# Optimization experiments

Measured on AMD Instinct MI355X. Metric: run time of the kernel, lower is better.

## Reference

```python
import jax, jax.numpy as jnp
import numpy as np

ALPHA = 0.2  # LeakyReLU negative slope


def setup_inputs() -> dict:
    key = jax.random.key(0)
    ks = jax.random.split(key, 6)
    B, N, F_in, F_out, H = 16, 1024, 256, 256, 8
    h = jax.random.normal(ks[0], (B, N, F_in), dtype=jnp.float32)
    # Per-head Linear W: weight [F_out, F_in] + bias [F_out], stacked over heads
    W = jax.random.normal(ks[1], (H, F_out, F_in), dtype=jnp.float32) * (1.414 / np.sqrt(F_in))
    bW = jax.random.normal(ks[2], (H, F_out), dtype=jnp.float32) * 0.01
    # Per-head Linear A: weight [1, 2*F_out] split into a1 (acts on Whi) and a2 (acts on Whj), bias bA [1]
    a1 = jax.random.normal(ks[3], (H, F_out), dtype=jnp.float32) * (1.414 / np.sqrt(2 * F_out))
    a2 = jax.random.normal(ks[4], (H, F_out), dtype=jnp.float32) * (1.414 / np.sqrt(2 * F_out))
    bA = jax.random.normal(ks[5], (H,), dtype=jnp.float32) * 0.01
    return {"h": h, "W": W, "bW": bW, "a1": a1, "a2": a2, "bA": bA}


def reference(h, W, bW, a1, a2, bA):
    # h: [B,N,F_in], W: [H,F_out,F_in]
    B, N, _ = h.shape
    H, F_out, _ = W.shape
    Wh = jnp.einsum('bnf,hof->bhno', h, W) + bW[None, :, None, :]  # [B,H,N,F_out]
    # Additive score e_ij = a1.Wh_i + a2.Wh_j + bA  (decomposed; avoids N x N x 2F concat)
    ei = jnp.einsum('bhno,ho->bhn', Wh, a1)  # contribution of row node i
    ej = jnp.einsum('bhno,ho->bhn', Wh, a2)  # contribution of col node j
    e = ei[:, :, :, None] + ej[:, :, None, :] + bA[None, :, None, None]  # [B,H,N,N]
    e = jnp.where(e > 0, e, ALPHA * e)  # LeakyReLU
    att = jax.nn.softmax(e, axis=-1)  # softmax over neighbors j (dropout = identity in eval)
    aWh = jnp.einsum('bhij,bhjo->bhio', att, Wh)  # [B,H,N,F_out]
    out = jax.nn.relu(aWh)  # last=False branch
    out = out.transpose(0, 2, 1, 3).reshape(B, N, H * F_out)  # concat heads on feature dim
    return jax.nn.sigmoid(out)
```

## Files before the change

### kernel.cpp

```cpp
#include <hip/hip_runtime.h>


#define L2E 1.442695041f

typedef _Float16 half8 __attribute__((ext_vector_type(8)));
typedef __fp16 fp16x2 __attribute__((ext_vector_type(2)));
typedef float floatx4 __attribute__((ext_vector_type(4)));

#if __has_builtin(__builtin_amdgcn_exp2f)
#define EXP2F(x) __builtin_amdgcn_exp2f(x)
#else
#define EXP2F(x) exp2f(x)
#endif

static __device__ inline unsigned int pack2(float a, float b) {
    fp16x2 h = __builtin_amdgcn_cvt_pkrtz(a, b);
    return __builtin_bit_cast(unsigned int, h);
}

static __device__ inline int swz(int row, int c) {
    return (row << 6) + ((((c) ^ (row >> 1)) & 3) << 4);
}
static __device__ inline int swz128(int row, int c) {
    return (row << 7) + ((((c) ^ row) & 7) << 4);
}

__global__ __launch_bounds__(256, 3) void wh_kernel(
    const float* __restrict__ hin, const float* __restrict__ W,
    const float* __restrict__ bW, _Float16* __restrict__ WhT,
    const float* __restrict__ a1, const float* __restrict__ a2,
    float* __restrict__ eiP, float* __restrict__ ejP)
{
    const int bnt  = blockIdx.x;
    const int ot   = blockIdx.y;
    const int head = blockIdx.z;
    const int t    = threadIdx.x;
    const int wave = t >> 6, lane = t & 63;
    const int l15 = lane & 15, quad = lane >> 4;
    const int wmh = wave & 1, wnh = wave >> 1;

    __shared__ char smem[16384];
    _Float16* As = (_Float16*)smem;
    _Float16* Bs = (_Float16*)(smem + 8192);
    float* bWs   = (float*)smem;
    float* a1s   = (float*)(smem + 512);
    float* a2s   = (float*)(smem + 1024);
    float* part1 = (float*)(smem + 1536);
    float* part2 = (float*)(smem + 2560);

    const int o0 = ot * 128;
    const int bn0 = bnt * 128;
    floatx4 acc[4][4];
#pragma unroll
    for (int a = 0; a < 4; a++)
#pragma unroll
        for (int b = 0; b < 4; b++) acc[a][b] = (floatx4)0.0f;

    const int ar = t >> 1, ah = t & 1;
    const float* Wrow = W + (size_t)(head * 256 + o0 + ar) * 256 + ah * 16;
    const float* hrow = hin + (size_t)(bn0 + ar) * 256 + ah * 16;

    float4 pa0, pa1, pa2, pa3, pb0, pb1, pb2, pb3;
    {
        const float4* p4 = (const float4*)Wrow;
        pa0 = p4[0]; pa1 = p4[1]; pa2 = p4[2]; pa3 = p4[3];
        const float4* q4 = (const float4*)hrow;
        pb0 = q4[0]; pb1 = q4[1]; pb2 = q4[2]; pb3 = q4[3];
    }

    for (int f0 = 0; f0 < 256; f0 += 32) {
        __syncthreads();
        *(uint4*)((char*)As + swz(ar, 2 * ah)) =
            make_uint4(pack2(pa0.x, pa0.y), pack2(pa0.z, pa0.w),
                       pack2(pa1.x, pa1.y), pack2(pa1.z, pa1.w));
        *(uint4*)((char*)As + swz(ar, 2 * ah + 1)) =
            make_uint4(pack2(pa2.x, pa2.y), pack2(pa2.z, pa2.w),
                       pack2(pa3.x, pa3.y), pack2(pa3.z, pa3.w));
        *(uint4*)((char*)Bs + swz(ar, 2 * ah)) =
            make_uint4(pack2(pb0.x, pb0.y), pack2(pb0.z, pb0.w),
                       pack2(pb1.x, pb1.y), pack2(pb1.z, pb1.w));
        *(uint4*)((char*)Bs + swz(ar, 2 * ah + 1)) =
            make_uint4(pack2(pb2.x, pb2.y), pack2(pb2.z, pb2.w),
                       pack2(pb3.x, pb3.y), pack2(pb3.z, pb3.w));
        if (f0 < 224) {
            const float4* p4 = (const float4*)(Wrow + f0 + 32);
            pa0 = p4[0]; pa1 = p4[1]; pa2 = p4[2]; pa3 = p4[3];
            const float4* q4 = (const float4*)(hrow + f0 + 32);
            pb0 = q4[0]; pb1 = q4[1]; pb2 = q4[2]; pb3 = q4[3];
        }
        __syncthreads();
        half8 af[4], bf[4];
#pragma unroll
        for (int a = 0; a < 4; a++)
            af[a] = *(const half8*)((char*)As + swz(wmh * 64 + a * 16 + l15, quad));
#pragma unroll
        for (int b = 0; b < 4; b++)
            bf[b] = *(const half8*)((char*)Bs + swz(wnh * 64 + b * 16 + l15, quad));
#pragma unroll
        for (int a = 0; a < 4; a++)
#pragma unroll
            for (int b = 0; b < 4; b++)
                acc[a][b] = __builtin_amdgcn_mfma_f32_16x16x32_f16(af[a], bf[b], acc[a][b], 0, 0, 0);
    }

    __syncthreads();
    if (t < 128) {
        bWs[t] = bW[head * 256 + o0 + t];
        a1s[t] = a1[head * 256 + o0 + t];
        a2s[t] = a2[head * 256 + o0 + t];
    }
    __syncthreads();

    const int bidx = bn0 >> 10;
    const int nbase = bn0 & 1023;
#pragma unroll
    for (int b = 0; b < 4; b++) {
        const int bnl = wnh * 64 + b * 16 + l15;
        const int n = nbase + bnl;
        float p1 = 0.f, p2 = 0.f;
#pragma unroll
        for (int a = 0; a < 4; a++) {
#pragma unroll
            for (int r = 0; r < 4; r++) {
                int ol = wmh * 64 + a * 16 + quad * 4 + r;
                float v = acc[a][b][r] + bWs[ol];
                WhT[(((size_t)(bidx * 8 + head) * 256 + o0 + ol) << 10) + n] = (_Float16)v;
                p1 = fmaf(v, a1s[ol], p1);
                p2 = fmaf(v, a2s[ol], p2);
            }
        }
        p1 += __shfl_xor(p1, 16, 64); p1 += __shfl_xor(p1, 32, 64);
        p2 += __shfl_xor(p2, 16, 64); p2 += __shfl_xor(p2, 32, 64);
        if (lane < 16) {
            part1[wmh * 128 + bnl] = p1;
            part2[wmh * 128 + bnl] = p2;
        }
    }
    __syncthreads();
    if (t < 128) {
        float s1 = part1[t] + part1[128 + t];
        float s2 = part2[t] + part2[128 + t];
        const size_t idx = (size_t)(bidx * 8 + head) * 1024 + nbase + t;
        eiP[(size_t)ot * 131072 + idx] = s1;
        ejP[(size_t)ot * 131072 + idx] = s2;
    }
}

__global__ __launch_bounds__(256, 3) void pv_kernel(
    const _Float16* __restrict__ WhT, const float* __restrict__ eiP,
    const float* __restrict__ ejP, const float* __restrict__ bA,
    float* __restrict__ out)
{
    const int bh = blockIdx.x;
    const int it = blockIdx.y;
    const int ot = blockIdx.z;
    const int b = bh >> 3, head = bh & 7;
    const int t = threadIdx.x;
    const int wave = t >> 6, lane = t & 63;
    const int l15 = lane & 15, quad = lane >> 4;
    const int wmh = wave & 1, wnh = wave >> 1;

    __shared__ char smem[37440];
    _Float16* Ap = (_Float16*)smem;
    _Float16* Bp = (_Float16*)(smem + 16384);
    float* ejs  = (float*)(smem + 32768);
    float* lns  = (float*)(smem + 36864);
    float* wred = (float*)(smem + 37376);

    const float* ej0 = ejP + bh * 1024;
    const float* ej1 = ejP + 131072 + bh * 1024;
    float mx = -1e30f;
#pragma unroll
    for (int k = 0; k < 4; k++) {
        int idx = t + k * 256;
        float v = (ej0[idx] + ej1[idx]) * L2E;
        ejs[idx] = v;
        mx = fmaxf(mx, v);
    }
#pragma unroll
    for (int m = 32; m; m >>= 1) mx = fmaxf(mx, __shfl_xor(mx, m, 64));
    if (lane == 0) wred[wave] = mx;
    __syncthreads();
    float ejmax = fmaxf(fmaxf(wred[0], wred[1]), fmaxf(wred[2], wred[3]));

    const int i0 = it * 128, o0 = ot * 128;
    const int prow = t >> 1, pjh = t & 1;
    const float cip = (eiP[bh * 1024 + i0 + prow] +
                       eiP[131072 + bh * 1024 + i0 + prow] + bA[head]) * L2E;
    const float tmv = cip + ejmax;
    const float nm = -fmaxf(tmv, 0.2f * tmv);

    const int wr_ = t >> 1, hh = t & 1;
    const _Float16* wrow = WhT + ((size_t)bh << 18) + ((size_t)(o0 + wr_) << 10) + hh * 32;

    floatx4 acc[4][4], accl[4];
#pragma unroll
    for (int a = 0; a < 4; a++) {
        accl[a] = (floatx4)0.0f;
#pragma unroll
        for (int c = 0; c < 4; c++) acc[a][c] = (floatx4)0.0f;
    }
    const bool doL = (wnh == 0);
    const half8 ones = {1, 1, 1, 1, 1, 1, 1, 1};

    uint4 w0, w1, w2, w3;
    { const uint4* s = (const uint4*)wrow; w0 = s[0]; w1 = s[1]; w2 = s[2]; w3 = s[3]; }

    for (int j0 = 0; j0 < 1024; j0 += 64) {
        __syncthreads();
        {
            const float4* ejp4 = (const float4*)(ejs + j0 + pjh * 32);
#pragma unroll
            for (int q = 0; q < 4; q++) {
                float4 e4a = ejp4[2 * q], e4b = ejp4[2 * q + 1];
                float p[8];
                const float ev[8] = {e4a.x, e4a.y, e4a.z, e4a.w,
                                     e4b.x, e4b.y, e4b.z, e4b.w};
#pragma unroll
                for (int u = 0; u < 8; u++) {
                    float e = cip + ev[u];
                    float lr = fmaxf(e, 0.2f * e);
                    p[u] = EXP2F(lr + nm);
                }
                *(uint4*)((char*)Ap + swz128(prow, pjh * 4 + q)) =
                    make_uint4(pack2(p[0], p[1]), pack2(p[2], p[3]),
                               pack2(p[4], p[5]), pack2(p[6], p[7]));
            }
        }
        {
            const int c0 = 4 * hh;
            *(uint4*)((char*)Bp + swz128(wr_, c0))     = w0;
            *(uint4*)((char*)Bp + swz128(wr_, c0 + 1)) = w1;
            *(uint4*)((char*)Bp + swz128(wr_, c0 + 2)) = w2;
            *(uint4*)((char*)Bp + swz128(wr_, c0 + 3)) = w3;
        }
        if (j0 < 960) {
            const uint4* s = (const uint4*)(wrow + j0 + 64);
            w0 = s[0]; w1 = s[1]; w2 = s[2]; w3 = s[3];
        }
        __syncthreads();
#pragma unroll
        for (int kk = 0; kk < 2; kk++) {
            half8 af[4], bf[4];
#pragma unroll
            for (int a = 0; a < 4; a++)
                af[a] = *(const half8*)((char*)Ap + swz128(wmh * 64 + a * 16 + l15, kk * 4 + quad));
#pragma unroll
            for (int c = 0; c < 4; c++)
                bf[c] = *(const half8*)((char*)Bp + swz128(wnh * 64 + c * 16 + l15, kk * 4 + quad));
            if (doL) {
#pragma unroll
                for (int a = 0; a < 4; a++)
                    accl[a] = __builtin_amdgcn_mfma_f32_16x16x32_f16(af[a], ones, accl[a], 0, 0, 0);
            }
#pragma unroll
            for (int a = 0; a < 4; a++)
#pragma unroll
                for (int c = 0; c < 4; c++)
                    acc[a][c] = __builtin_amdgcn_mfma_f32_16x16x32_f16(af[a], bf[c], acc[a][c], 0, 0, 0);
        }
    }

    __syncthreads();
    if (doL && l15 == 0) {
#pragma unroll
        for (int a = 0; a < 4; a++)
#pragma unroll
            for (int r = 0; r < 4; r++)
                lns[wmh * 64 + a * 16 + quad * 4 + r] = accl[a][r];
    }
    __syncthreads();

    float rinv[4][4];
#pragma unroll
    for (int a = 0; a < 4; a++)
#pragma unroll
        for (int r = 0; r < 4; r++)
            rinv[a][r] = 1.0f / lns[wmh * 64 + a * 16 + quad * 4 + r];

#pragma unroll
    for (int a = 0; a < 4; a++) {
#pragma unroll
        for (int c = 0; c < 4; c++) {
            int o = o0 + wnh * 64 + c * 16 + l15;
#pragma unroll
            for (int r = 0; r < 4; r++) {
                int i = i0 + wmh * 64 + a * 16 + quad * 4 + r;
                float v = acc[a][c][r] * rinv[a][r];
                float rl = fmaxf(v, 0.0f);
                float y = 1.0f / (1.0f + EXP2F(-rl * L2E));
                out[((size_t)(b * 1024 + i) << 11) + head * 256 + o] = y;
            }
        }
    }
}

extern "C" void kernel_launch(void* const* d_in, const int* in_sizes, int n_in,
                              void* d_out, int out_size, void* d_ws, size_t ws_size,
                              hipStream_t stream)
{
    const float* h  = (const float*)d_in[0];
    const float* W  = (const float*)d_in[1];
    const float* bW = (const float*)d_in[2];
    const float* a1 = (const float*)d_in[3];
    const float* a2 = (const float*)d_in[4];
    const float* bA = (const float*)d_in[5];
    float* out = (float*)d_out;

    char* ws = (char*)d_ws;
    _Float16* WhT = (_Float16*)ws;
    float* eiP = (float*)(ws + 67108864);
    float* ejP = (float*)(ws + 67108864 + 1048576);

    hipLaunchKernelGGL(wh_kernel, dim3(128, 2, 8), dim3(256), 0, stream,
                       h, W, bW, WhT, a1, a2, eiP, ejP);
    hipLaunchKernelGGL(pv_kernel, dim3(128, 8, 2), dim3(256), 0, stream,
                       WhT, eiP, ejP, bA, out);
}
```

Measured before the change: 296.0 us.

## Widen pv tile to full 256 output features and load Wh via global_load_lds

The pv kernel now covers all 256 output columns per block instead of splitting them across two blocks. This halves the redundant recomputation of the exp/softmax attention tile (A operand). The Wh tile is now copied straight from global memory into LDS with the global_load_lds builtin and an XOR swizzle, replacing the register-staged prefetch. The cost is a doubled accumulator register footprint, larger LDS use, and occupancy lowered to 2 blocks. The direct-to-LDS load is issued in the same iteration it is consumed, so its latency is no longer hidden by a prefetch one step ahead.

```diff
diff --git a/kernel.cpp b/kernel.cpp
--- a/kernel.cpp
+++ b/kernel.cpp
@@ -16,6 +16,12 @@
 static __device__ inline unsigned int pack2(float a, float b) {
     fp16x2 h = __builtin_amdgcn_cvt_pkrtz(a, b);
     return __builtin_bit_cast(unsigned int, h);
+}
+
+typedef __attribute__((address_space(1))) const void GV;
+typedef __attribute__((address_space(3))) void LV;
+static __device__ inline void load_lds16(const void* g, void* l) {
+    __builtin_amdgcn_global_load_lds((GV*)g, (LV*)l, 16, 0, 0);
 }
 
 static __device__ inline int swz(int row, int c) {
@@ -146,26 +152,25 @@
     }
 }
 
-__global__ __launch_bounds__(256, 3) void pv_kernel(
+__global__ __launch_bounds__(256, 2) void pv_kernel(
     const _Float16* __restrict__ WhT, const float* __restrict__ eiP,
     const float* __restrict__ ejP, const float* __restrict__ bA,
     float* __restrict__ out)
 {
     const int bh = blockIdx.x;
     const int it = blockIdx.y;
-    const int ot = blockIdx.z;
     const int b = bh >> 3, head = bh & 7;
     const int t = threadIdx.x;
     const int wave = t >> 6, lane = t & 63;
     const int l15 = lane & 15, quad = lane >> 4;
     const int wmh = wave & 1, wnh = wave >> 1;
 
-    __shared__ char smem[37440];
+    __shared__ char smem[53776];
     _Float16* Ap = (_Float16*)smem;
     _Float16* Bp = (_Float16*)(smem + 16384);
-    float* ejs  = (float*)(smem + 32768);
-    float* lns  = (float*)(smem + 36864);
-    float* wred = (float*)(smem + 37376);
+    float* ejs  = (float*)(smem + 49152);
+    float* lns  = (float*)(smem + 53248);
+    float* wred = (float*)(smem + 53760);
 
     const float* ej0 = ejP + bh * 1024;
     const float* ej1 = ejP + 131072 + bh * 1024;
@@ -183,31 +188,34 @@
     __syncthreads();
     float ejmax = fmaxf(fmaxf(wred[0], wred[1]), fmaxf(wred[2], wred[3]));
 
-    const int i0 = it * 128, o0 = ot * 128;
+    const int i0 = it * 128;
     const int prow = t >> 1, pjh = t & 1;
     const float cip = (eiP[bh * 1024 + i0 + prow] +
                        eiP[131072 + bh * 1024 + i0 + prow] + bA[head]) * L2E;
     const float tmv = cip + ejmax;
     const float nm = -fmaxf(tmv, 0.2f * tmv);
 
-    const int wr_ = t >> 1, hh = t & 1;
-    const _Float16* wrow = WhT + ((size_t)bh << 18) + ((size_t)(o0 + wr_) << 10) + hh * 32;
-
-    floatx4 acc[4][4], accl[4];
+    const int rsub = lane >> 3, cp7 = lane & 7;
+    const _Float16* bsrc = WhT + ((size_t)bh << 18)
+                         + ((size_t)(wave * 64 + rsub) << 10)
+                         + ((cp7 ^ rsub) << 3);
+    char* bdst0 = (char*)Bp + wave * 8192;
+
+    floatx4 acc[4][8], accl[4];
 #pragma unroll
     for (int a = 0; a < 4; a++) {
         accl[a] = (floatx4)0.0f;
 #pragma unroll
-        for (int c = 0; c < 4; c++) acc[a][c] = (floatx4)0.0f;
+        for (int c = 0; c < 8; c++) acc[a][c] = (floatx4)0.0f;
     }
     const bool doL = (wnh == 0);
     const half8 ones = {1, 1, 1, 1, 1, 1, 1, 1};
 
-    uint4 w0, w1, w2, w3;
-    { const uint4* s = (const uint4*)wrow; w0 = s[0]; w1 = s[1]; w2 = s[2]; w3 = s[3]; }
-
     for (int j0 = 0; j0 < 1024; j0 += 64) {
         __syncthreads();
+#pragma unroll
+        for (int q = 0; q < 8; q++)
+            load_lds16(bsrc + j0 + q * 8192, bdst0 + q * 1024);
         {
             const float4* ejp4 = (const float4*)(ejs + j0 + pjh * 32);
 #pragma unroll
@@ -227,27 +235,16 @@
                                pack2(p[4], p[5]), pack2(p[6], p[7]));
             }
         }
-        {
-            const int c0 = 4 * hh;
-            *(uint4*)((char*)Bp + swz128(wr_, c0))     = w0;
-            *(uint4*)((char*)Bp + swz128(wr_, c0 + 1)) = w1;
-            *(uint4*)((char*)Bp + swz128(wr_, c0 + 2)) = w2;
-            *(uint4*)((char*)Bp + swz128(wr_, c0 + 3)) = w3;
-        }
-        if (j0 < 960) {
-            const uint4* s = (const uint4*)(wrow + j0 + 64);
-            w0 = s[0]; w1 = s[1]; w2 = s[2]; w3 = s[3];
-        }
         __syncthreads();
 #pragma unroll
         for (int kk = 0; kk < 2; kk++) {
-            half8 af[4], bf[4];
+            half8 af[4], bf[8];
 #pragma unroll
             for (int a = 0; a < 4; a++)
                 af[a] = *(const half8*)((char*)Ap + swz128(wmh * 64 + a * 16 + l15, kk * 4 + quad));
 #pragma unroll
-            for (int c = 0; c < 4; c++)
-                bf[c] = *(const half8*)((char*)Bp + swz128(wnh * 64 + c * 16 + l15, kk * 4 + quad));
+            for (int c = 0; c < 8; c++)
+                bf[c] = *(const half8*)((char*)Bp + swz128(wnh * 128 + c * 16 + l15, kk * 4 + quad));
             if (doL) {
 #pragma unroll
                 for (int a = 0; a < 4; a++)
@@ -256,7 +253,7 @@
 #pragma unroll
             for (int a = 0; a < 4; a++)
 #pragma unroll
-                for (int c = 0; c < 4; c++)
+                for (int c = 0; c < 8; c++)
                     acc[a][c] = __builtin_amdgcn_mfma_f32_16x16x32_f16(af[a], bf[c], acc[a][c], 0, 0, 0);
         }
     }
@@ -281,8 +278,8 @@
 #pragma unroll
     for (int a = 0; a < 4; a++) {
 #pragma unroll
-        for (int c = 0; c < 4; c++) {
-            int o = o0 + wnh * 64 + c * 16 + l15;
+        for (int c = 0; c < 8; c++) {
+            int o = wnh * 128 + c * 16 + l15;
 #pragma unroll
             for (int r = 0; r < 4; r++) {
                 int i = i0 + wmh * 64 + a * 16 + quad * 4 + r;
@@ -314,6 +311,6 @@
 
     hipLaunchKernelGGL(wh_kernel, dim3(128, 2, 8), dim3(256), 0, stream,
                        h, W, bW, WhT, a1, a2, eiP, ejP);
-    hipLaunchKernelGGL(pv_kernel, dim3(128, 8, 2), dim3(256), 0, stream,
+    hipLaunchKernelGGL(pv_kernel, dim3(128, 8), dim3(256), 0, stream,
                        WhT, eiP, ejP, bA, out);
 }
```

Measured after the change: 280.8 us. -5.1%, faster.
